# Kernel optimization log

Measured on AMD Instinct MI355X. Metric: run time of the kernel, lower is better.

The kernel has to match this reference:

```python
import jax, jax.numpy as jnp
import numpy as np

IN_FEATURES = 4096
OUT_FEATURES = 11008
BLOCK_SIZE = 64

NF4_TABLE = jnp.array([-1.0, -0.6961928009986877, -0.5250730514526367, -0.39491748809814453,
                       -0.28444138169288635, -0.18477343022823334, -0.09105003625154495, 0.0,
                       0.07958029955625534, 0.16093020141124725, 0.24611230194568634,
                       0.33791524171829224, 0.44070982933044434, 0.5626170039176941,
                       0.7229568362236023, 1.0], dtype=jnp.float32)


def setup_inputs() -> dict:
    key = jax.random.key(0)
    k1, k2, k3, k4 = jax.random.split(key, 4)
    n = IN_FEATURES * OUT_FEATURES
    x = jax.random.normal(k1, (4, 128, IN_FEATURES), dtype=jnp.float32)
    # packed 4-bit codes: two codes per byte, flat layout as produced by quantize_and_pack_nf4
    packed_kernel = jax.random.randint(k2, (n // 2,), 0, 256, dtype=jnp.int32).astype(jnp.uint8)
    # per-block absmax scales (positive)
    scales = jax.random.uniform(k3, (n // BLOCK_SIZE,), minval=0.01, maxval=0.05, dtype=jnp.float32)
    bias = jax.random.normal(k4, (OUT_FEATURES,), dtype=jnp.float32) * 0.01
    return {"x": x, "packed_kernel": packed_kernel, "scales": scales, "bias": bias}


def _dequantize_nf4(packed, absmax, block_size):
    high = (packed >> 4) & 15
    low = packed & 15
    # interleave: [h0, l0, h1, l1, ...] matching jnp.stack([high, low], axis=1).reshape(-1)
    unpacked = jnp.stack([high, low], axis=1).reshape(-1)
    deq = NF4_TABLE[unpacked]                       # [n] fp32
    deq = deq.reshape(-1, block_size) * absmax[:, None]  # per-block scaling
    return deq


def reference(x, packed_kernel, scales, bias):
    kernel = _dequantize_nf4(packed_kernel, scales, BLOCK_SIZE).reshape(IN_FEATURES, OUT_FEATURES)
    y = jnp.einsum("bsi,io->bso", x, kernel)
    y = y + bias
    return y
```

## Files before the change

kernel.cpp:

```cpp
#include <hip/hip_runtime.h>
#include <hip/hip_bf16.h>
#include <hip/hip_fp16.h>
#include <stdint.h>

#define K_DIM 4096
#define N_DIM 11008
#define M_DIM 512
#define PK_ROW 5504
#define SC_ROW 172

typedef __attribute__((ext_vector_type(4))) float f32x4;
typedef __attribute__((ext_vector_type(4))) int i32x4;
typedef __attribute__((ext_vector_type(4))) unsigned int u32x4;
typedef __attribute__((ext_vector_type(8))) _Float16 half8;
typedef __attribute__((ext_vector_type(8))) short bf16x8;

__constant__ float NF4[16] = {
    -1.0f, -0.6961928009986877f, -0.5250730514526367f, -0.39491748809814453f,
    -0.28444138169288635f, -0.18477343022823334f, -0.09105003625154495f, 0.0f,
    0.07958029955625534f, 0.16093020141124725f, 0.24611230194568634f,
    0.33791524171829224f, 0.44070982933044434f, 0.5626170039176941f,
    0.7229568362236023f, 1.0f};

union H8 { u32x4 v; half8 h; };

__device__ __forceinline__ unsigned h2mul(unsigned a, unsigned b) {
  union { __half2 h; unsigned u; } x, y, r;
  x.u = a; y.u = b;
  r.h = x.h * y.h;
  return r.u;
}
__device__ __forceinline__ unsigned hpack(float a, float b) {
  union { __half2 h; unsigned u; } c;
  c.h = __floats2half2_rn(a, b);
  return c.u;
}
__device__ __forceinline__ unsigned f2bf(float v) {
  union { __hip_bfloat16 h; unsigned short u; } cv;
  cv.h = __float2bfloat16(v);
  return (unsigned)cv.u;
}

__global__ __launch_bounds__(256) void prep_all(
    const float* __restrict__ x, const int* __restrict__ packed,
    const float* __restrict__ scales, unsigned* __restrict__ wsa,
    unsigned* __restrict__ codes, unsigned* __restrict__ scalesp) {
  const int bid = blockIdx.x;
  const int t = threadIdx.x;
  if (bid < 5504) {
    const int kt = bid & 63;
    const int nt = bid >> 6;
    __shared__ unsigned char Sb[128 * 36];
    const int npl = t & 63;
    const int kq = t >> 6;
    const int np = nt * 64 + npl;
#pragma unroll
    for (int i = 0; i < 8; ++i) {
      const int kpl = kq + i * 4;
      const int k = kt * 64 + kpl * 2;
      const int w0 = packed[(size_t)k * PK_ROW + np];
      const int w1 = packed[(size_t)(k + 1) * PK_ROW + np];
      Sb[(npl * 2) * 36 + kpl] =
          (unsigned char)((((w0 >> 4) & 15) << 4) | ((w1 >> 4) & 15));
      Sb[(npl * 2 + 1) * 36 + kpl] =
          (unsigned char)(((w0 & 15) << 4) | (w1 & 15));
    }
    __syncthreads();
#pragma unroll
    for (int i = 0; i < 4; ++i) {
      const int lin = t + 256 * i;
      const int n16 = lin & 15;
      const int kp4l = (lin >> 4) & 7;
      const int nb16l = lin >> 7;
      const unsigned v = *(const unsigned*)(Sb + (nb16l * 16 + n16) * 36 + kp4l * 4);
      const size_t D = ((size_t)(nt * 8 + nb16l) * 512 + kt * 8 + kp4l) * 16 + n16;
      codes[D] = v;
    }
  } else if (bid < 6528) {
    const int wid = (bid - 5504) * 4 + (t >> 6);
    const int lane = t & 63;
    const int m16 = wid >> 7, k32 = wid & 127;
    const int m = m16 * 16 + (lane & 15);
    const int k = k32 * 32 + (lane >> 4) * 8;
    const float* src = x + (size_t)m * K_DIM + k;
    f32x4 v0 = *(const f32x4*)src;
    f32x4 v1 = *(const f32x4*)(src + 4);
    u32x4 d;
    d[0] = hpack(v0[0], v0[1]);
    d[1] = hpack(v0[2], v0[3]);
    d[2] = hpack(v1[0], v1[1]);
    d[3] = hpack(v1[2], v1[3]);
    *(u32x4*)(wsa + (size_t)wid * 256 + lane * 4) = d;
  } else {
    const int g = (bid - 6528) * 256 + t;
    if (g < SC_ROW * 2048) {
      const int kp = g / SC_ROW;
      const int nb = g - kp * SC_ROW;
      const float s0 = scales[(size_t)(2 * kp) * SC_ROW + nb];
      const float s1 = scales[(size_t)(2 * kp + 1) * SC_ROW + nb];
      scalesp[(size_t)nb * 2048 + kp] = hpack(s0, s1);
    }
  }
}

__global__ __launch_bounds__(256, 3) void nf4_gemm_ib(
    const unsigned* __restrict__ codes, const unsigned* __restrict__ scalesp,
    const unsigned* __restrict__ wsa, const float* __restrict__ bias,
    float* __restrict__ out) {
  __shared__ unsigned LutR[256 * 32];
  __shared__ __align__(16) float Red[2][2][64][20];

  const int bid = blockIdx.x;
  const int x = bid & 7;
  const int local = bid >> 3;
  const int S = (x < 6) ? x * 11 : 66 + (x - 6) * 10;
  const int cnt = (x < 6) ? 11 : 10;
  if (local >= cnt * 8) return;
  const int n_tile = (S + (local >> 3)) * 128;
  const int m_tile = (local & 7) * 64;

  const int t = threadIdx.x;
  {
    const int c = t & 31;
    const int b0 = t >> 5;
#pragma unroll
    for (int i = 0; i < 32; ++i) {
      const int b = b0 + 8 * i;
      LutR[b * 32 + c] = hpack(NF4[(b >> 4) & 15], NF4[b & 15]);
    }
  }
  __syncthreads();

  const int lane = t & 63;
  const int wid = t >> 6;
  const int kh = wid >> 1;
  const int nh = wid & 1;
  const int l15 = lane & 15;
  const int kslice = lane >> 4;
  const int lb = lane & 31;
  const int m16w = m_tile >> 4;
  const int nf0 = (n_tile >> 4) + nh * 4;
  const int nb64 = (n_tile >> 6) + nh;

  unsigned cb[4];
#pragma unroll
  for (int j = 0; j < 4; ++j) cb[j] = (unsigned)(nf0 + j) * 8192 + lane;
  const unsigned sb = (unsigned)nb64 * 2048 + kslice * 4;
  unsigned ab[4];
#pragma unroll
  for (int fm = 0; fm < 4; ++fm)
    ab[fm] = (unsigned)(m16w + fm) * 32768 + lane * 4;

  f32x4 acc[4][4];
#pragma unroll
  for (int i = 0; i < 4; ++i)
#pragma unroll
    for (int j = 0; j < 4; ++j) acc[i][j] = (f32x4){0.f, 0.f, 0.f, 0.f};

  const int NS = 64;
  const int s_base = kh * NS;

  auto LOAD = [&](int sl, unsigned* c, u32x4& sv, u32x4* A) {
    const unsigned s = (unsigned)(s_base + sl);
#pragma unroll
    for (int j = 0; j < 4; ++j) c[j] = codes[cb[j] + 64u * s];
    sv = *(const u32x4*)(scalesp + sb + 16u * s);
#pragma unroll
    for (int fm = 0; fm < 4; ++fm)
      A[fm] = *(const u32x4*)(wsa + ab[fm] + 256u * s);
  };
  auto STEP = [&](const unsigned* c, const u32x4& sv, const u32x4* A) {
    H8 a[4];
#pragma unroll
    for (int fm = 0; fm < 4; ++fm) a[fm].v = A[fm];
#pragma unroll
    for (int j = 0; j < 4; ++j) {
      const unsigned cw = c[j];
      H8 B;
      B.v[0] = h2mul(LutR[((cw & 255u) << 5) | lb], sv[0]);
      B.v[1] = h2mul(LutR[(((cw >> 8) & 255u) << 5) | lb], sv[1]);
      B.v[2] = h2mul(LutR[(((cw >> 16) & 255u) << 5) | lb], sv[2]);
      B.v[3] = h2mul(LutR[((cw >> 24) << 5) | lb], sv[3]);
#pragma unroll
      for (int fm = 0; fm < 4; ++fm)
        acc[fm][j] = __builtin_amdgcn_mfma_f32_16x16x32_f16(a[fm].h, B.h, acc[fm][j], 0, 0, 0);
    }
  };

  unsigned Xc[4], Yc[4];
  u32x4 Xs, Ys;
  u32x4 XA[4], YA[4];
  LOAD(0, Xc, Xs, XA);
#pragma unroll 1
  for (int s = 0; s < NS; s += 2) {
    LOAD(s + 1, Yc, Ys, YA);
    STEP(Xc, Xs, XA);
    if (s + 2 < NS) LOAD(s + 2, Xc, Xs, XA);
    STEP(Yc, Ys, YA);
  }

#pragma unroll 1
  for (int jr = 0; jr < 2; ++jr) {
    if (kh == 1) {
#pragma unroll
      for (int jj = 0; jj < 2; ++jj)
#pragma unroll
        for (int fm = 0; fm < 4; ++fm)
          *(f32x4*)&Red[jj][nh][lane][fm * 4] = acc[fm][jr * 2 + jj];
    }
    __syncthreads();
    if (kh == 0) {
#pragma unroll
      for (int jj = 0; jj < 2; ++jj) {
        const int j = jr * 2 + jj;
        const int gc = n_tile + nh * 64 + j * 16 + l15;
        const float bi = bias[gc];
#pragma unroll
        for (int fm = 0; fm < 4; ++fm) {
          const f32x4 o = acc[fm][j] + *(const f32x4*)&Red[jj][nh][lane][fm * 4];
#pragma unroll
          for (int r = 0; r < 4; ++r) {
            const int gr = m_tile + fm * 16 + kslice * 4 + r;
            out[(size_t)gr * N_DIM + gc] = o[r] + bi;
          }
        }
      }
    }
    __syncthreads();
  }
}

#define FLDS 72
__global__ __launch_bounds__(256) void nf4_gemm_fused(
    const float* __restrict__ x, const int* __restrict__ packed,
    const float* __restrict__ scales, const float* __restrict__ bias,
    float* __restrict__ out) {
  __shared__ unsigned short AldsF[128 * FLDS];
  __shared__ unsigned short BldsF[128 * FLDS];
  __shared__ float2 Lut[256];
  const int t = threadIdx.x;
  const int bid = blockIdx.x;
  const int swz = (bid & 7) * 43 + (bid >> 3);
  const int m_tile = (swz / 86) * 128;
  const int n_tile = (swz % 86) * 128;
  Lut[t] = make_float2(NF4[(t >> 4) & 15], NF4[t & 15]);
  const int lane = t & 63;
  const int wid = t >> 6;
  const int wm = (wid >> 1) * 64;
  const int wn = (wid & 1) * 64;
  const int l15 = lane & 15;
  const int l4 = lane >> 4;
  f32x4 acc[4][4];
#pragma unroll
  for (int i = 0; i < 4; ++i)
#pragma unroll
    for (int j = 0; j < 4; ++j) acc[i][j] = (f32x4){0.f, 0.f, 0.f, 0.f};
  const int mlane = t & 15;
  const int n_sub = mlane * 8;
  const int k_sub = 4 * (((t >> 4) + mlane) & 15);
  const int c4 = t & 15;
  const int r0 = t >> 4;
  for (int k0 = 0; k0 < K_DIM; k0 += 64) {
    __syncthreads();
#pragma unroll
    for (int i = 0; i < 8; ++i) {
      const int row = r0 + 16 * i;
      f32x4 xv = *(const f32x4*)(x + (size_t)(m_tile + row) * K_DIM + k0 + c4 * 4);
      uint2 d;
      d.x = f2bf(xv[0]) | (f2bf(xv[1]) << 16);
      d.y = f2bf(xv[2]) | (f2bf(xv[3]) << 16);
      *(uint2*)(&AldsF[row * FLDS + c4 * 4]) = d;
    }
    {
      const int* pk = packed + (size_t)(k0 + k_sub) * PK_ROW + ((n_tile + n_sub) >> 1);
      i32x4 w[4];
      float s[4];
#pragma unroll
      for (int kk = 0; kk < 4; ++kk) {
        w[kk] = *(const i32x4*)(pk + (size_t)kk * PK_ROW);
        s[kk] = scales[(size_t)(k0 + k_sub + kk) * SC_ROW + ((n_tile + n_sub) >> 6)];
      }
      float v[4][8];
#pragma unroll
      for (int kk = 0; kk < 4; ++kk)
#pragma unroll
        for (int e = 0; e < 4; ++e) {
          const int b = w[kk][e] & 0xFF;
          const float2 p = Lut[b];
          v[kk][2 * e] = p.x * s[kk];
          v[kk][2 * e + 1] = p.y * s[kk];
        }
#pragma unroll
      for (int j = 0; j < 8; ++j) {
        uint2 d;
        d.x = f2bf(v[0][j]) | (f2bf(v[1][j]) << 16);
        d.y = f2bf(v[2][j]) | (f2bf(v[3][j]) << 16);
        *(uint2*)(&BldsF[(n_sub + j) * FLDS + k_sub]) = d;
      }
    }
    __syncthreads();
#pragma unroll
    for (int ks = 0; ks < 2; ++ks) {
      bf16x8 af[4], bfv[4];
#pragma unroll
      for (int fm = 0; fm < 4; ++fm)
        af[fm] = *(const bf16x8*)(&AldsF[(wm + fm * 16 + l15) * FLDS + ks * 32 + l4 * 8]);
#pragma unroll
      for (int fn = 0; fn < 4; ++fn)
        bfv[fn] = *(const bf16x8*)(&BldsF[(wn + fn * 16 + l15) * FLDS + ks * 32 + l4 * 8]);
#pragma unroll
      for (int fm = 0; fm < 4; ++fm)
#pragma unroll
        for (int fn = 0; fn < 4; ++fn)
          acc[fm][fn] = __builtin_amdgcn_mfma_f32_16x16x32_bf16(af[fm], bfv[fn], acc[fm][fn], 0, 0, 0);
    }
  }
#pragma unroll
  for (int fn = 0; fn < 4; ++fn) {
    const float bi = bias[n_tile + wn + fn * 16 + l15];
#pragma unroll
    for (int fm = 0; fm < 4; ++fm)
#pragma unroll
      for (int r = 0; r < 4; ++r) {
        const int gr = m_tile + wm + fm * 16 + l4 * 4 + r;
        out[(size_t)gr * N_DIM + n_tile + wn + fn * 16 + l15] = acc[fm][fn][r] + bi;
      }
  }
}

extern "C" void kernel_launch(void* const* d_in, const int* in_sizes, int n_in,
                              void* d_out, int out_size, void* d_ws, size_t ws_size,
                              hipStream_t stream) {
  const float* x = (const float*)d_in[0];
  const int* packed = (const int*)d_in[1];
  const float* scales = (const float*)d_in[2];
  const float* bias = (const float*)d_in[3];
  float* out = (float*)d_out;

  const size_t A_BYTES = (size_t)M_DIM * K_DIM * 2;
  const size_t C_BYTES = (size_t)688 * 512 * 16 * 4;
  const size_t S_BYTES = (size_t)SC_ROW * 2048 * 4;
  const size_t need = A_BYTES + C_BYTES + S_BYTES;

  if (ws_size >= need) {
    unsigned* wsa = (unsigned*)d_ws;
    unsigned* codes = (unsigned*)((char*)d_ws + A_BYTES);
    unsigned* scalesp = (unsigned*)((char*)d_ws + A_BYTES + C_BYTES);
    prep_all<<<dim3(7904), dim3(256), 0, stream>>>(x, packed, scales, wsa, codes, scalesp);
    nf4_gemm_ib<<<dim3(704), dim3(256), 0, stream>>>(codes, scalesp, wsa, bias, out);
  } else {
    nf4_gemm_fused<<<dim3(344), dim3(256), 0, stream>>>(x, packed, scales, bias, out);
  }
}
```

Before: 97.74 us.

## Stage output tile in LDS for coalesced vector stores; shrink replicated LUT

Cuts the replicated NF4 byte-pair lookup table in shared memory from 32 to 16 copies. The split-K reduction epilogue now writes the second K-half's accumulators into a full 64x128 fp32 LDS tile. The first half then adds its partials plus bias in place, and all four waves write the tile out with 16-byte coalesced row stores instead of scattered 4-byte stores. This removes uncoalesced global writes and one barrier round. The cost is more LDS traffic with possible bank conflicts in the LUT lookups, and a larger LDS footprint that may affect occupancy.

```diff
diff --git a/kernel.cpp b/kernel.cpp
--- a/kernel.cpp
+++ b/kernel.cpp
@@ -107,8 +107,8 @@
     const unsigned* __restrict__ codes, const unsigned* __restrict__ scalesp,
     const unsigned* __restrict__ wsa, const float* __restrict__ bias,
     float* __restrict__ out) {
-  __shared__ unsigned LutR[256 * 32];
-  __shared__ __align__(16) float Red[2][2][64][20];
+  __shared__ unsigned LutR[256 * 16];
+  __shared__ __align__(16) float Otile[64][132];
 
   const int bid = blockIdx.x;
   const int x = bid & 7;
@@ -121,12 +121,12 @@
 
   const int t = threadIdx.x;
   {
-    const int c = t & 31;
-    const int b0 = t >> 5;
-#pragma unroll
-    for (int i = 0; i < 32; ++i) {
-      const int b = b0 + 8 * i;
-      LutR[b * 32 + c] = hpack(NF4[(b >> 4) & 15], NF4[b & 15]);
+    const int c = t & 15;
+    const int b0 = t >> 4;
+#pragma unroll
+    for (int i = 0; i < 16; ++i) {
+      const int b = b0 + 16 * i;
+      LutR[b * 16 + c] = hpack(NF4[(b >> 4) & 15], NF4[b & 15]);
     }
   }
   __syncthreads();
@@ -137,7 +137,7 @@
   const int nh = wid & 1;
   const int l15 = lane & 15;
   const int kslice = lane >> 4;
-  const int lb = lane & 31;
+  const int lb = lane & 15;
   const int m16w = m_tile >> 4;
   const int nf0 = (n_tile >> 4) + nh * 4;
   const int nb64 = (n_tile >> 6) + nh;
@@ -177,10 +177,10 @@
     for (int j = 0; j < 4; ++j) {
       const unsigned cw = c[j];
       H8 B;
-      B.v[0] = h2mul(LutR[((cw & 255u) << 5) | lb], sv[0]);
-      B.v[1] = h2mul(LutR[(((cw >> 8) & 255u) << 5) | lb], sv[1]);
-      B.v[2] = h2mul(LutR[(((cw >> 16) & 255u) << 5) | lb], sv[2]);
-      B.v[3] = h2mul(LutR[((cw >> 24) << 5) | lb], sv[3]);
+      B.v[0] = h2mul(LutR[((cw & 255u) << 4) | lb], sv[0]);
+      B.v[1] = h2mul(LutR[(((cw >> 8) & 255u) << 4) | lb], sv[1]);
+      B.v[2] = h2mul(LutR[(((cw >> 16) & 255u) << 4) | lb], sv[2]);
+      B.v[3] = h2mul(LutR[((cw >> 24) << 4) | lb], sv[3]);
 #pragma unroll
       for (int fm = 0; fm < 4; ++fm)
         acc[fm][j] = __builtin_amdgcn_mfma_f32_16x16x32_f16(a[fm].h, B.h, acc[fm][j], 0, 0, 0);
@@ -199,34 +199,40 @@
     STEP(Yc, Ys, YA);
   }
 
-#pragma unroll 1
-  for (int jr = 0; jr < 2; ++jr) {
-    if (kh == 1) {
-#pragma unroll
-      for (int jj = 0; jj < 2; ++jj)
-#pragma unroll
-        for (int fm = 0; fm < 4; ++fm)
-          *(f32x4*)&Red[jj][nh][lane][fm * 4] = acc[fm][jr * 2 + jj];
-    }
-    __syncthreads();
-    if (kh == 0) {
-#pragma unroll
-      for (int jj = 0; jj < 2; ++jj) {
-        const int j = jr * 2 + jj;
-        const int gc = n_tile + nh * 64 + j * 16 + l15;
-        const float bi = bias[gc];
-#pragma unroll
-        for (int fm = 0; fm < 4; ++fm) {
-          const f32x4 o = acc[fm][j] + *(const f32x4*)&Red[jj][nh][lane][fm * 4];
-#pragma unroll
-          for (int r = 0; r < 4; ++r) {
-            const int gr = m_tile + fm * 16 + kslice * 4 + r;
-            out[(size_t)gr * N_DIM + gc] = o[r] + bi;
-          }
+  if (kh == 1) {
+#pragma unroll
+    for (int j = 0; j < 4; ++j)
+#pragma unroll
+      for (int fm = 0; fm < 4; ++fm)
+#pragma unroll
+        for (int r = 0; r < 4; ++r)
+          Otile[fm * 16 + kslice * 4 + r][nh * 64 + j * 16 + l15] = acc[fm][j][r];
+  }
+  __syncthreads();
+  if (kh == 0) {
+#pragma unroll
+    for (int j = 0; j < 4; ++j) {
+      const float bi = bias[n_tile + nh * 64 + j * 16 + l15];
+#pragma unroll
+      for (int fm = 0; fm < 4; ++fm)
+#pragma unroll
+        for (int r = 0; r < 4; ++r) {
+          const int row = fm * 16 + kslice * 4 + r;
+          const int col = nh * 64 + j * 16 + l15;
+          Otile[row][col] += acc[fm][j][r] + bi;
         }
-      }
-    }
-    __syncthreads();
+    }
+  }
+  __syncthreads();
+  {
+    const int c8 = lane & 31;
+    const int r2 = lane >> 5;
+#pragma unroll
+    for (int it = 0; it < 8; ++it) {
+      const int row = it * 8 + wid * 2 + r2;
+      const f32x4 v = *(const f32x4*)&Otile[row][c8 * 4];
+      *(f32x4*)&out[(size_t)(m_tile + row) * N_DIM + n_tile + c8 * 4] = v;
+    }
   }
 }
 
```

New measurement: 83.14 us, median of 2. -14.9%, faster.
